# Performance work log

Measured on AMD Instinct MI355X. Metric: run time of the kernel, lower is better.

## Reference

```python
import jax, jax.numpy as jnp
import numpy as np

H, W = 256, 256
S, S_IDX, END_BIAS = 48, 3, 10
E_IDX = S - END_BIAS          # 38
N_ITER = E_IDX - (S_IDX + 1)  # 34 sequential segments after the start segment
OUT_WIN = 10                  # outlier1d window length
OUT_THRESH = 2.0


def setup_inputs() -> dict:
    key = jax.random.key(0)
    # (x, y) event coordinates in [0, W) x [0, H); t/p/b columns are unused by the module.
    events = jax.random.uniform(key, (16, 960000, 2), jnp.float32, minval=0.0, maxval=256.0)
    return {"events": events}


def _blur(a):
    """5x5 uniform (0.04) blur, SAME padding; a: [B, S, D] -> [B, S, D]."""
    k = jnp.full((1, 1, 5, 5), 0.04, jnp.float32)
    return jax.lax.conv_general_dilated(a[:, None], k, (1, 1), [(2, 2), (2, 2)])[:, 0]


def _outlier_flags(m):
    """outlier1d(m[b, si:si+10], thresh=2)[0] for si in [S_IDX+1, E_IDX). m: [B,S] -> bool [B,N_ITER]."""
    widx = (jnp.arange(N_ITER)[:, None] + S_IDX + 1) + jnp.arange(OUT_WIN)[None, :]
    w = m[:, widx]                                   # [B, N_ITER, 10]
    med = jnp.median(w, axis=-1, keepdims=True)
    diff = jnp.abs(w - med)
    mad = jnp.median(diff, axis=-1)                  # [B, N_ITER]
    return 0.6745 * diff[..., 0] / mad > OUT_THRESH


def reference(events):
    B, N, _ = events.shape
    segmentLen = N // S            # static python int
    Nu = segmentLen * S
    x = events[:, :Nu, 0].astype(jnp.int32)   # [B, Nu]
    y = events[:, :Nu, 1].astype(jnp.int32)
    chunks = jnp.repeat(jnp.arange(S), segmentLen)   # segment id per event, [Nu]
    bidx = jnp.arange(B)[:, None]

    # per-batch x-t / y-t histograms via scatter-add
    alongX = jnp.zeros((B, S, W), jnp.float32).at[bidx, chunks[None, :], x].add(1.0)
    alongY = jnp.zeros((B, S, H), jnp.float32).at[bidx, chunks[None, :], y].add(1.0)

    def proc_axis(along, D):
        flat = along.reshape(B, -1)
        cv = (flat.mean(-1) + 3.0 * jnp.std(flat, axis=-1, ddof=1))[:, None, None]
        a = _blur(jnp.clip(along, 0.0, cv))
        m = jnp.einsum('bsd,d->bs', a, jnp.arange(D, dtype=jnp.float32)) / segmentLen
        start = m[:, S_IDX:S_IDX + 1]
        aligned = jnp.round(m - start - (D // 2 - start)).astype(jnp.int32)
        return m, aligned

    meanX, alignedX = proc_axis(alongX, W)
    meanY, alignedY = proc_axis(alongY, H)
    is_out = _outlier_flags(meanX) | _outlier_flags(meanY)   # [B, N_ITER]

    def per_batch(xb, yb, aX, aY, outb):
        xs = jnp.clip(xb - aX[chunks], 0, W - 1)
        ys = jnp.clip(yb - aY[chunks], 0, H - 1)
        idx_c = (xs + W * ys).reshape(S, segmentLen)
        idx_v = (xs // 2 + (W // 2) * (ys // 2)).reshape(S, segmentLen)
        container0 = jnp.zeros(W * H, jnp.int32).at[idx_c[S_IDX]].add(1)
        ver0 = jnp.zeros((W // 2) * (H // 2), bool).at[idx_v[S_IDX]].set(True)

        def step(carry, inp):
            container, ver, stopped = carry
            ic, iv, is_o = inp
            ver_new = ver.at[iv].set(True)
            cnt = jnp.sum(ver_new).astype(jnp.float32)
            new_info = jnp.sum(jnp.logical_xor(ver_new, ver)).astype(jnp.float32)
            brk = new_info / cnt < 0.1
            do = (~stopped) & (~is_o) & (~brk)
            stopped = stopped | ((~stopped) & (~is_o) & brk)
            container = jnp.where(do, container.at[ic].add(1), container)
            ver = jnp.where(do, ver_new, ver)
            return (container, ver, stopped), None

        (container, _, _), _ = jax.lax.scan(
            step, (container0, ver0, jnp.array(False)),
            (idx_c[S_IDX + 1:E_IDX], idx_v[S_IDX + 1:E_IDX], outb))
        c = container.astype(jnp.float32)
        cv = c.mean() + 3.0 * jnp.std(c, ddof=1)
        return jnp.clip(c, 0.0, cv) / cv

    containers = jax.vmap(per_batch)(x, y, alignedX, alignedY, is_out)  # [B, W*H]
    return containers.reshape(B, 1, H, W)
```

## Files before the change

### kernel.cpp

```cpp
#include <hip/hip_runtime.h>

#define NB 16
#define NEV 960000
#define NS 48
#define SEG 20000
#define S_IDX 3
#define E_IDX 38
#define N_ITER 34
#define ND 256
#define NCH 35

__global__ __launch_bounds__(256) void hist_kernel(const float* __restrict__ events,
                                                   float* __restrict__ alongX,
                                                   float* __restrict__ alongY,
                                                   unsigned* __restrict__ compact,
                                                   unsigned* __restrict__ container,
                                                   unsigned* __restrict__ masks,
                                                   unsigned long long* __restrict__ sums,
                                                   unsigned long long* __restrict__ cvsums) {
    __shared__ unsigned hx[4][ND], hy[4][ND];
    __shared__ unsigned long long qredX[4], qredY[4];
    int tid = threadIdx.x;
    int blk = blockIdx.x;
    int b = blk / NS, c = blk % NS;
    int wave = tid >> 6, lane = tid & 63;
    #pragma unroll
    for (int j = 0; j < 4; j++) { hx[j][tid] = 0; hy[j][tid] = 0; }
    {
        uint4 z = {0u, 0u, 0u, 0u};
        for (int i = blk * 256 + tid; i < 262144; i += NB * NS * 256)
            ((uint4*)container)[i] = z;
        for (int i = blk * 256 + tid; i < 71680; i += NB * NS * 256)
            ((uint4*)masks)[i] = z;
        if (blk == 0 && tid < NB * 2) sums[tid] = 0ull;
        if (blk == 1 && tid < NB * 2) cvsums[tid] = 0ull;
    }
    __syncthreads();
    size_t base = (size_t)b * NEV + (size_t)c * SEG;
    const float4* ev4 = (const float4*)(events + base * 2);
    bool wr = (c >= S_IDX && c < E_IDX);
    uint4* dst = wr ? (uint4*)(compact + ((size_t)b * NCH + (c - S_IDX)) * (SEG / 2)) : nullptr;
    unsigned* HX = hx[wave];
    unsigned* HY = hy[wave];
    for (int k = tid; k < SEG / 8; k += 256) {
        float4 v0 = ev4[4 * k], v1 = ev4[4 * k + 1], v2 = ev4[4 * k + 2], v3 = ev4[4 * k + 3];
        int x0 = (int)v0.x, y0 = (int)v0.y, x1 = (int)v0.z, y1 = (int)v0.w;
        int x2 = (int)v1.x, y2 = (int)v1.y, x3 = (int)v1.z, y3 = (int)v1.w;
        int x4 = (int)v2.x, y4 = (int)v2.y, x5 = (int)v2.z, y5 = (int)v2.w;
        int x6 = (int)v3.x, y6 = (int)v3.y, x7 = (int)v3.z, y7 = (int)v3.w;
        x0 = x0 > 255 ? 255 : x0; y0 = y0 > 255 ? 255 : y0;
        x1 = x1 > 255 ? 255 : x1; y1 = y1 > 255 ? 255 : y1;
        x2 = x2 > 255 ? 255 : x2; y2 = y2 > 255 ? 255 : y2;
        x3 = x3 > 255 ? 255 : x3; y3 = y3 > 255 ? 255 : y3;
        x4 = x4 > 255 ? 255 : x4; y4 = y4 > 255 ? 255 : y4;
        x5 = x5 > 255 ? 255 : x5; y5 = y5 > 255 ? 255 : y5;
        x6 = x6 > 255 ? 255 : x6; y6 = y6 > 255 ? 255 : y6;
        x7 = x7 > 255 ? 255 : x7; y7 = y7 > 255 ? 255 : y7;
        atomicAdd(&HX[x0], 1u); atomicAdd(&HY[y0], 1u);
        atomicAdd(&HX[x1], 1u); atomicAdd(&HY[y1], 1u);
        atomicAdd(&HX[x2], 1u); atomicAdd(&HY[y2], 1u);
        atomicAdd(&HX[x3], 1u); atomicAdd(&HY[y3], 1u);
        atomicAdd(&HX[x4], 1u); atomicAdd(&HY[y4], 1u);
        atomicAdd(&HX[x5], 1u); atomicAdd(&HY[y5], 1u);
        atomicAdd(&HX[x6], 1u); atomicAdd(&HY[y6], 1u);
        atomicAdd(&HX[x7], 1u); atomicAdd(&HY[y7], 1u);
        if (wr) {
            uint4 p;
            p.x = (unsigned)(x0 | (y0 << 8)) | ((unsigned)(x1 | (y1 << 8)) << 16);
            p.y = (unsigned)(x2 | (y2 << 8)) | ((unsigned)(x3 | (y3 << 8)) << 16);
            p.z = (unsigned)(x4 | (y4 << 8)) | ((unsigned)(x5 | (y5 << 8)) << 16);
            p.w = (unsigned)(x6 | (y6 << 8)) | ((unsigned)(x7 | (y7 << 8)) << 16);
            dst[k] = p;
        }
    }
    __syncthreads();
    unsigned sx = hx[0][tid] + hx[1][tid] + hx[2][tid] + hx[3][tid];
    unsigned sy = hy[0][tid] + hy[1][tid] + hy[2][tid] + hy[3][tid];
    int o = (b * NS + c) * ND + tid;
    alongX[o] = (float)sx;
    alongY[o] = (float)sy;
    unsigned long long qx = (unsigned long long)sx * sx;
    unsigned long long qy = (unsigned long long)sy * sy;
    for (int off = 32; off; off >>= 1) { qx += __shfl_down(qx, off); qy += __shfl_down(qy, off); }
    if (lane == 0) { qredX[wave] = qx; qredY[wave] = qy; }
    __syncthreads();
    if (tid == 0) {
        atomicAdd(&cvsums[b * 2],     qredX[0] + qredX[1] + qredX[2] + qredX[3]);
        atomicAdd(&cvsums[b * 2 + 1], qredY[0] + qredY[1] + qredY[2] + qredY[3]);
    }
}

__global__ __launch_bounds__(256) void stats_kernel(const float* __restrict__ alongX,
                                                    const float* __restrict__ alongY,
                                                    const unsigned long long* __restrict__ cvsums,
                                                    int* __restrict__ alignedX,
                                                    int* __restrict__ alignedY,
                                                    float* __restrict__ m_all) {
    __shared__ float sbuf[16 * ND];
    int tid = threadIdx.x;
    int blk = blockIdx.x;
    int g = blk & 3, axis = (blk >> 2) & 1, b = blk >> 3;
    const float* along = (axis ? alongY : alongX) + (size_t)b * NS * ND;
    int rbase = g * 12 - 2;
    for (int j = 0; j < 16; j++) {
        int r = rbase + j;
        if (r >= 0 && r < NS) sbuf[j * ND + tid] = along[r * ND + tid];
    }
    double ts  = 960000.0;
    double ts2 = (double)cvsums[b * 2 + axis];
    const double N = (double)(NS * ND);
    double mean = ts / N;
    double var  = (ts2 - ts * ts / N) / (N - 1.0);
    float cv = (float)(mean + 3.0 * sqrt(var));
    __syncthreads();
    int wave = tid >> 6, lane = tid & 63;
    for (int q = 0; q < 3; ++q) {
        int sI = g * 12 + wave * 3 + q;
        double acc = 0.0;
        #pragma unroll
        for (int k = 0; k < 4; ++k) {
            int d = lane + 64 * k;
            int lo = d - 2 < 0 ? 0 : d - 2;
            int hi = d + 2 > 255 ? 255 : d + 2;
            double Wd = 0.5 * (double)(lo + hi) * (double)(hi - lo + 1);
            double t = 0.0;
            #pragma unroll
            for (int ds = -2; ds <= 2; ++ds) {
                int ss = sI + ds;
                if (ss >= 0 && ss < NS) t += (double)fminf(sbuf[(ss - rbase) * ND + d], cv);
            }
            acc += t * Wd;
        }
        for (int off = 32; off; off >>= 1) acc += __shfl_down(acc, off);
        if (lane == 0) {
            float mf = (float)(acc * 0.04 / (double)SEG);
            m_all[(b * 2 + axis) * NS + sI] = mf;
            (axis ? alignedY : alignedX)[b * NS + sI] = (int)rintf(mf - 128.0f);
        }
    }
}

__global__ __launch_bounds__(256) void mask_kernel(const unsigned* __restrict__ compact,
                                                   const int* __restrict__ alignedX,
                                                   const int* __restrict__ alignedY,
                                                   unsigned* __restrict__ masks) {
    __shared__ unsigned sm[512];
    int tid = threadIdx.x, blk = blockIdx.x;
    int hi = blk & 1;
    int tile = blk >> 1;
    int b = tile / NCH, ci = tile % NCH, si = S_IDX + ci;
    sm[tid] = 0; sm[tid + 256] = 0;
    __syncthreads();
    int aX = alignedX[b * NS + si], aY = alignedY[b * NS + si];
    const uint4* cp = (const uint4*)(compact + ((size_t)b * NCH + ci) * (SEG / 2));
    for (int i = hi * 1250 + tid; i < (hi + 1) * 1250; i += 256) {
        uint4 w = cp[i];
        unsigned wsv[4] = {w.x, w.y, w.z, w.w};
        #pragma unroll
        for (int j = 0; j < 4; j++) {
            unsigned v = wsv[j];
            #pragma unroll
            for (int h = 0; h < 2; h++) {
                unsigned e = (h ? (v >> 16) : v) & 0xFFFFu;
                int xs = (int)(e & 255u) - aX; xs = xs < 0 ? 0 : (xs > 255 ? 255 : xs);
                int ys = (int)(e >> 8)   - aY; ys = ys < 0 ? 0 : (ys > 255 ? 255 : ys);
                int iv = (xs >> 1) | ((ys >> 1) << 7);
                atomicOr(&sm[iv >> 5], 1u << (iv & 31));
            }
        }
    }
    __syncthreads();
    unsigned* mo = masks + (size_t)tile * 512;
    unsigned v0 = sm[tid], v1 = sm[tid + 256];
    if (v0) atomicOr(&mo[tid], v0);
    if (v1) atomicOr(&mo[tid + 256], v1);
}

__device__ inline float median10(const float* v) {
    float w[10];
    #pragma unroll
    for (int i = 0; i < 10; i++) w[i] = v[i];
    #pragma unroll
    for (int i = 1; i < 10; i++) {
        float k = w[i]; int j = i - 1;
        while (j >= 0 && w[j] > k) { w[j + 1] = w[j]; j--; }
        w[j + 1] = k;
    }
    return 0.5f * (w[4] + w[5]);
}

__device__ inline bool outlier_flag(const float* w) {
    float med = median10(w);
    float d[10];
    #pragma unroll
    for (int i = 0; i < 10; i++) d[i] = fabsf(w[i] - med);
    float d0 = d[0];
    float mad = median10(d);
    return (0.6745f * d0 / mad) > 2.0f;
}

__device__ inline unsigned wave_sum_u32(unsigned v) {
    for (int off = 32; off; off >>= 1) v += __shfl_xor(v, off);
    return v;
}

__global__ __launch_bounds__(64) void decide_kernel(const unsigned* __restrict__ masks,
                                                    const float* __restrict__ m_all,
                                                    unsigned long long* __restrict__ commitmask) {
    int b = blockIdx.x, lane = threadIdx.x;
    const unsigned* mb = masks + (size_t)b * NCH * 512;
    uint4 v0 = ((const uint4*)mb)[lane * 2];
    uint4 v1 = ((const uint4*)mb)[lane * 2 + 1];
    const uint4* pp = (const uint4*)(mb + 512);
    uint4 p0 = pp[lane * 2], p1 = pp[lane * 2 + 1];
    bool f = false;
    if (lane < N_ITER) {
        const float* mx = m_all + b * 2 * NS;
        const float* my = mx + NS;
        f = outlier_flag(&mx[S_IDX + 1 + lane]) || outlier_flag(&my[S_IDX + 1 + lane]);
    }
    unsigned long long omask = __ballot(f);
    unsigned ver[8] = {v0.x, v0.y, v0.z, v0.w, v1.x, v1.y, v1.z, v1.w};
    unsigned pc = 0;
    #pragma unroll
    for (int j = 0; j < 8; j++) pc += __popc(ver[j]);
    unsigned cnt = wave_sum_u32(pc);
    unsigned long long cm = 1ull;
    for (int idx = 1; idx < NCH; ++idx) {
        uint4 c0 = p0, c1 = p1;
        if (idx + 1 < NCH) {
            const uint4* np = (const uint4*)(mb + (size_t)(idx + 1) * 512);
            p0 = np[lane * 2]; p1 = np[lane * 2 + 1];
        }
        unsigned del[8] = {c0.x, c0.y, c0.z, c0.w, c1.x, c1.y, c1.z, c1.w};
        unsigned nl = 0;
        #pragma unroll
        for (int j = 0; j < 8; j++) nl += __popc(del[j] & ~ver[j]);
        unsigned ni = wave_sum_u32(nl);
        bool is_o = (omask >> (idx - 1)) & 1;
        if (!is_o) {
            unsigned cn = cnt + ni;
            float ratio = (float)ni / (float)cn;
            if (ratio < 0.1f) break;
            cm |= 1ull << idx;
            cnt = cn;
            #pragma unroll
            for (int j = 0; j < 8; j++) ver[j] |= del[j];
        }
    }
    if (lane == 0) commitmask[b] = cm;
}

__global__ __launch_bounds__(256) void commit_kernel(const unsigned* __restrict__ compact,
                                                     const int* __restrict__ alignedX,
                                                     const int* __restrict__ alignedY,
                                                     const unsigned long long* __restrict__ commitmask,
                                                     unsigned* __restrict__ container) {
    int blk = blockIdx.x, tid = threadIdx.x;
    int qi = blk & 3;
    int tile = blk >> 2;
    int b = tile / NCH, ci = tile % NCH;
    if (!((commitmask[b] >> ci) & 1ull)) return;
    int si = S_IDX + ci;
    int aX = alignedX[b * NS + si], aY = alignedY[b * NS + si];
    unsigned* cont = container + (size_t)b * 65536;
    const uint4* cp = (const uint4*)(compact + ((size_t)b * NCH + ci) * (SEG / 2));
    for (int i = qi * 625 + tid; i < (qi + 1) * 625; i += 256) {
        uint4 w = cp[i];
        unsigned wsv[4] = {w.x, w.y, w.z, w.w};
        #pragma unroll
        for (int j = 0; j < 4; j++) {
            unsigned v = wsv[j];
            #pragma unroll
            for (int h = 0; h < 2; h++) {
                unsigned e = (h ? (v >> 16) : v) & 0xFFFFu;
                int xs = (int)(e & 255u) - aX; xs = xs < 0 ? 0 : (xs > 255 ? 255 : xs);
                int ys = (int)(e >> 8)   - aY; ys = ys < 0 ? 0 : (ys > 255 ? 255 : ys);
                atomicAdd(&cont[xs | (ys << 8)], 1u);
            }
        }
    }
}

__global__ __launch_bounds__(256) void cv_kernel(const unsigned* __restrict__ container,
                                                 unsigned long long* __restrict__ sums) {
    __shared__ unsigned long long sredA[4], sredB[4];
    int tid = threadIdx.x, blk = blockIdx.x;
    int b = blk >> 4, part = blk & 15;
    const uint4* c4 = (const uint4*)(container + (size_t)b * 65536) + part * 1024;
    unsigned long long s = 0, s2 = 0;
    for (int i = tid; i < 1024; i += 256) {
        uint4 v = c4[i];
        s  += (unsigned long long)v.x + v.y + v.z + v.w;
        s2 += (unsigned long long)v.x * v.x + (unsigned long long)v.y * v.y
            + (unsigned long long)v.z * v.z + (unsigned long long)v.w * v.w;
    }
    for (int off = 32; off; off >>= 1) { s += __shfl_down(s, off); s2 += __shfl_down(s2, off); }
    if ((tid & 63) == 0) { sredA[tid >> 6] = s; sredB[tid >> 6] = s2; }
    __syncthreads();
    if (tid == 0) {
        atomicAdd(&sums[b * 2],     sredA[0] + sredA[1] + sredA[2] + sredA[3]);
        atomicAdd(&sums[b * 2 + 1], sredB[0] + sredB[1] + sredB[2] + sredB[3]);
    }
}

__global__ __launch_bounds__(256) void finish_kernel(const unsigned* __restrict__ container,
                                                     const unsigned long long* __restrict__ sums,
                                                     float* __restrict__ out) {
    int g = blockIdx.x * 256 + threadIdx.x;
    int b = g >> 14;
    double ts  = (double)sums[b * 2];
    double ts2 = (double)sums[b * 2 + 1];
    double mean = ts / 65536.0;
    double var  = (ts2 - ts * ts / 65536.0) / 65535.0;
    float cv = (float)(mean + 3.0 * sqrt(var));
    uint4 v = ((const uint4*)container)[g];
    float4 o;
    o.x = fminf((float)v.x, cv) / cv;
    o.y = fminf((float)v.y, cv) / cv;
    o.z = fminf((float)v.z, cv) / cv;
    o.w = fminf((float)v.w, cv) / cv;
    ((float4*)out)[g] = o;
}

extern "C" void kernel_launch(void* const* d_in, const int* in_sizes, int n_in,
                              void* d_out, int out_size, void* d_ws, size_t ws_size,
                              hipStream_t stream) {
    const float* events = (const float*)d_in[0];
    float* out = (float*)d_out;
    char* ws = (char*)d_ws;

    float*    alongX    = (float*)(ws);
    float*    alongY    = (float*)(ws + 786432);
    unsigned* container = (unsigned*)(ws + 1572864);
    int*      alignedX  = (int*)(ws + 5767168);
    int*      alignedY  = (int*)(ws + 5770240);
    float*    m_all     = (float*)(ws + 5773312);
    unsigned long long* commitmask = (unsigned long long*)(ws + 5779456);
    unsigned long long* sums       = (unsigned long long*)(ws + 5779584);
    unsigned long long* cvsums     = (unsigned long long*)(ws + 5779840);
    unsigned* compact   = (unsigned*)(ws + 6291456);
    unsigned* masks     = (unsigned*)(ws + 29360128);

    hist_kernel<<<NB * NS, 256, 0, stream>>>(events, alongX, alongY, compact,
                                             container, masks, sums, cvsums);
    stats_kernel<<<NB * 2 * 4, 256, 0, stream>>>(alongX, alongY, cvsums,
                                                 alignedX, alignedY, m_all);
    mask_kernel<<<NB * NCH * 2, 256, 0, stream>>>(compact, alignedX, alignedY, masks);
    decide_kernel<<<NB, 64, 0, stream>>>(masks, m_all, commitmask);
    commit_kernel<<<NB * NCH * 4, 256, 0, stream>>>(compact, alignedX, alignedY,
                                                    commitmask, container);
    cv_kernel<<<NB * 16, 256, 0, stream>>>(container, sums);
    finish_kernel<<<1024, 256, 0, stream>>>(container, sums, out);
}
```

Before: 269.4 us.

## Fuse all seven pipeline kernels into one cooperative persistent kernel with grid syncs

Replaces the seven separate kernel launches with a single cooperative mega-kernel of 768 blocks. Stages are separated by grid.sync(), and shared memory is reused through a union. The aim is to remove per-launch overhead and inter-kernel gaps, which matter here because several stages are tiny. In exchange the grid is fixed at 768 blocks, so some stages now loop over virtual blocks, and the many grid-wide barriers add their own synchronisation cost.

After: 841.5 us. 212% more time.

```diff
diff --git a/kernel.cpp b/kernel.cpp
--- a/kernel.cpp
+++ b/kernel.cpp
@@ -1,4 +1,7 @@
 #include <hip/hip_runtime.h>
+#include <hip/hip_cooperative_groups.h>
+
+namespace cg = cooperative_groups;
 
 #define NB 16
 #define NEV 960000
@@ -9,172 +12,7 @@
 #define N_ITER 34
 #define ND 256
 #define NCH 35
-
-__global__ __launch_bounds__(256) void hist_kernel(const float* __restrict__ events,
-                                                   float* __restrict__ alongX,
-                                                   float* __restrict__ alongY,
-                                                   unsigned* __restrict__ compact,
-                                                   unsigned* __restrict__ container,
-                                                   unsigned* __restrict__ masks,
-                                                   unsigned long long* __restrict__ sums,
-                                                   unsigned long long* __restrict__ cvsums) {
-    __shared__ unsigned hx[4][ND], hy[4][ND];
-    __shared__ unsigned long long qredX[4], qredY[4];
-    int tid = threadIdx.x;
-    int blk = blockIdx.x;
-    int b = blk / NS, c = blk % NS;
-    int wave = tid >> 6, lane = tid & 63;
-    #pragma unroll
-    for (int j = 0; j < 4; j++) { hx[j][tid] = 0; hy[j][tid] = 0; }
-    {
-        uint4 z = {0u, 0u, 0u, 0u};
-        for (int i = blk * 256 + tid; i < 262144; i += NB * NS * 256)
-            ((uint4*)container)[i] = z;
-        for (int i = blk * 256 + tid; i < 71680; i += NB * NS * 256)
-            ((uint4*)masks)[i] = z;
-        if (blk == 0 && tid < NB * 2) sums[tid] = 0ull;
-        if (blk == 1 && tid < NB * 2) cvsums[tid] = 0ull;
-    }
-    __syncthreads();
-    size_t base = (size_t)b * NEV + (size_t)c * SEG;
-    const float4* ev4 = (const float4*)(events + base * 2);
-    bool wr = (c >= S_IDX && c < E_IDX);
-    uint4* dst = wr ? (uint4*)(compact + ((size_t)b * NCH + (c - S_IDX)) * (SEG / 2)) : nullptr;
-    unsigned* HX = hx[wave];
-    unsigned* HY = hy[wave];
-    for (int k = tid; k < SEG / 8; k += 256) {
-        float4 v0 = ev4[4 * k], v1 = ev4[4 * k + 1], v2 = ev4[4 * k + 2], v3 = ev4[4 * k + 3];
-        int x0 = (int)v0.x, y0 = (int)v0.y, x1 = (int)v0.z, y1 = (int)v0.w;
-        int x2 = (int)v1.x, y2 = (int)v1.y, x3 = (int)v1.z, y3 = (int)v1.w;
-        int x4 = (int)v2.x, y4 = (int)v2.y, x5 = (int)v2.z, y5 = (int)v2.w;
-        int x6 = (int)v3.x, y6 = (int)v3.y, x7 = (int)v3.z, y7 = (int)v3.w;
-        x0 = x0 > 255 ? 255 : x0; y0 = y0 > 255 ? 255 : y0;
-        x1 = x1 > 255 ? 255 : x1; y1 = y1 > 255 ? 255 : y1;
-        x2 = x2 > 255 ? 255 : x2; y2 = y2 > 255 ? 255 : y2;
-        x3 = x3 > 255 ? 255 : x3; y3 = y3 > 255 ? 255 : y3;
-        x4 = x4 > 255 ? 255 : x4; y4 = y4 > 255 ? 255 : y4;
-        x5 = x5 > 255 ? 255 : x5; y5 = y5 > 255 ? 255 : y5;
-        x6 = x6 > 255 ? 255 : x6; y6 = y6 > 255 ? 255 : y6;
-        x7 = x7 > 255 ? 255 : x7; y7 = y7 > 255 ? 255 : y7;
-        atomicAdd(&HX[x0], 1u); atomicAdd(&HY[y0], 1u);
-        atomicAdd(&HX[x1], 1u); atomicAdd(&HY[y1], 1u);
-        atomicAdd(&HX[x2], 1u); atomicAdd(&HY[y2], 1u);
-        atomicAdd(&HX[x3], 1u); atomicAdd(&HY[y3], 1u);
-        atomicAdd(&HX[x4], 1u); atomicAdd(&HY[y4], 1u);
-        atomicAdd(&HX[x5], 1u); atomicAdd(&HY[y5], 1u);
-        atomicAdd(&HX[x6], 1u); atomicAdd(&HY[y6], 1u);
-        atomicAdd(&HX[x7], 1u); atomicAdd(&HY[y7], 1u);
-        if (wr) {
-            uint4 p;
-            p.x = (unsigned)(x0 | (y0 << 8)) | ((unsigned)(x1 | (y1 << 8)) << 16);
-            p.y = (unsigned)(x2 | (y2 << 8)) | ((unsigned)(x3 | (y3 << 8)) << 16);
-            p.z = (unsigned)(x4 | (y4 << 8)) | ((unsigned)(x5 | (y5 << 8)) << 16);
-            p.w = (unsigned)(x6 | (y6 << 8)) | ((unsigned)(x7 | (y7 << 8)) << 16);
-            dst[k] = p;
-        }
-    }
-    __syncthreads();
-    unsigned sx = hx[0][tid] + hx[1][tid] + hx[2][tid] + hx[3][tid];
-    unsigned sy = hy[0][tid] + hy[1][tid] + hy[2][tid] + hy[3][tid];
-    int o = (b * NS + c) * ND + tid;
-    alongX[o] = (float)sx;
-    alongY[o] = (float)sy;
-    unsigned long long qx = (unsigned long long)sx * sx;
-    unsigned long long qy = (unsigned long long)sy * sy;
-    for (int off = 32; off; off >>= 1) { qx += __shfl_down(qx, off); qy += __shfl_down(qy, off); }
-    if (lane == 0) { qredX[wave] = qx; qredY[wave] = qy; }
-    __syncthreads();
-    if (tid == 0) {
-        atomicAdd(&cvsums[b * 2],     qredX[0] + qredX[1] + qredX[2] + qredX[3]);
-        atomicAdd(&cvsums[b * 2 + 1], qredY[0] + qredY[1] + qredY[2] + qredY[3]);
-    }
-}
-
-__global__ __launch_bounds__(256) void stats_kernel(const float* __restrict__ alongX,
-                                                    const float* __restrict__ alongY,
-                                                    const unsigned long long* __restrict__ cvsums,
-                                                    int* __restrict__ alignedX,
-                                                    int* __restrict__ alignedY,
-                                                    float* __restrict__ m_all) {
-    __shared__ float sbuf[16 * ND];
-    int tid = threadIdx.x;
-    int blk = blockIdx.x;
-    int g = blk & 3, axis = (blk >> 2) & 1, b = blk >> 3;
-    const float* along = (axis ? alongY : alongX) + (size_t)b * NS * ND;
-    int rbase = g * 12 - 2;
-    for (int j = 0; j < 16; j++) {
-        int r = rbase + j;
-        if (r >= 0 && r < NS) sbuf[j * ND + tid] = along[r * ND + tid];
-    }
-    double ts  = 960000.0;
-    double ts2 = (double)cvsums[b * 2 + axis];
-    const double N = (double)(NS * ND);
-    double mean = ts / N;
-    double var  = (ts2 - ts * ts / N) / (N - 1.0);
-    float cv = (float)(mean + 3.0 * sqrt(var));
-    __syncthreads();
-    int wave = tid >> 6, lane = tid & 63;
-    for (int q = 0; q < 3; ++q) {
-        int sI = g * 12 + wave * 3 + q;
-        double acc = 0.0;
-        #pragma unroll
-        for (int k = 0; k < 4; ++k) {
-            int d = lane + 64 * k;
-            int lo = d - 2 < 0 ? 0 : d - 2;
-            int hi = d + 2 > 255 ? 255 : d + 2;
-            double Wd = 0.5 * (double)(lo + hi) * (double)(hi - lo + 1);
-            double t = 0.0;
-            #pragma unroll
-            for (int ds = -2; ds <= 2; ++ds) {
-                int ss = sI + ds;
-                if (ss >= 0 && ss < NS) t += (double)fminf(sbuf[(ss - rbase) * ND + d], cv);
-            }
-            acc += t * Wd;
-        }
-        for (int off = 32; off; off >>= 1) acc += __shfl_down(acc, off);
-        if (lane == 0) {
-            float mf = (float)(acc * 0.04 / (double)SEG);
-            m_all[(b * 2 + axis) * NS + sI] = mf;
-            (axis ? alignedY : alignedX)[b * NS + sI] = (int)rintf(mf - 128.0f);
-        }
-    }
-}
-
-__global__ __launch_bounds__(256) void mask_kernel(const unsigned* __restrict__ compact,
-                                                   const int* __restrict__ alignedX,
-                                                   const int* __restrict__ alignedY,
-                                                   unsigned* __restrict__ masks) {
-    __shared__ unsigned sm[512];
-    int tid = threadIdx.x, blk = blockIdx.x;
-    int hi = blk & 1;
-    int tile = blk >> 1;
-    int b = tile / NCH, ci = tile % NCH, si = S_IDX + ci;
-    sm[tid] = 0; sm[tid + 256] = 0;
-    __syncthreads();
-    int aX = alignedX[b * NS + si], aY = alignedY[b * NS + si];
-    const uint4* cp = (const uint4*)(compact + ((size_t)b * NCH + ci) * (SEG / 2));
-    for (int i = hi * 1250 + tid; i < (hi + 1) * 1250; i += 256) {
-        uint4 w = cp[i];
-        unsigned wsv[4] = {w.x, w.y, w.z, w.w};
-        #pragma unroll
-        for (int j = 0; j < 4; j++) {
-            unsigned v = wsv[j];
-            #pragma unroll
-            for (int h = 0; h < 2; h++) {
-                unsigned e = (h ? (v >> 16) : v) & 0xFFFFu;
-                int xs = (int)(e & 255u) - aX; xs = xs < 0 ? 0 : (xs > 255 ? 255 : xs);
-                int ys = (int)(e >> 8)   - aY; ys = ys < 0 ? 0 : (ys > 255 ? 255 : ys);
-                int iv = (xs >> 1) | ((ys >> 1) << 7);
-                atomicOr(&sm[iv >> 5], 1u << (iv & 31));
-            }
-        }
-    }
-    __syncthreads();
-    unsigned* mo = masks + (size_t)tile * 512;
-    unsigned v0 = sm[tid], v1 = sm[tid + 256];
-    if (v0) atomicOr(&mo[tid], v0);
-    if (v1) atomicOr(&mo[tid + 256], v1);
-}
+#define GRID 768
 
 __device__ inline float median10(const float* v) {
     float w[10];
@@ -204,132 +42,9 @@
     return v;
 }
 
-__global__ __launch_bounds__(64) void decide_kernel(const unsigned* __restrict__ masks,
-                                                    const float* __restrict__ m_all,
-                                                    unsigned long long* __restrict__ commitmask) {
-    int b = blockIdx.x, lane = threadIdx.x;
-    const unsigned* mb = masks + (size_t)b * NCH * 512;
-    uint4 v0 = ((const uint4*)mb)[lane * 2];
-    uint4 v1 = ((const uint4*)mb)[lane * 2 + 1];
-    const uint4* pp = (const uint4*)(mb + 512);
-    uint4 p0 = pp[lane * 2], p1 = pp[lane * 2 + 1];
-    bool f = false;
-    if (lane < N_ITER) {
-        const float* mx = m_all + b * 2 * NS;
-        const float* my = mx + NS;
-        f = outlier_flag(&mx[S_IDX + 1 + lane]) || outlier_flag(&my[S_IDX + 1 + lane]);
-    }
-    unsigned long long omask = __ballot(f);
-    unsigned ver[8] = {v0.x, v0.y, v0.z, v0.w, v1.x, v1.y, v1.z, v1.w};
-    unsigned pc = 0;
-    #pragma unroll
-    for (int j = 0; j < 8; j++) pc += __popc(ver[j]);
-    unsigned cnt = wave_sum_u32(pc);
-    unsigned long long cm = 1ull;
-    for (int idx = 1; idx < NCH; ++idx) {
-        uint4 c0 = p0, c1 = p1;
-        if (idx + 1 < NCH) {
-            const uint4* np = (const uint4*)(mb + (size_t)(idx + 1) * 512);
-            p0 = np[lane * 2]; p1 = np[lane * 2 + 1];
-        }
-        unsigned del[8] = {c0.x, c0.y, c0.z, c0.w, c1.x, c1.y, c1.z, c1.w};
-        unsigned nl = 0;
-        #pragma unroll
-        for (int j = 0; j < 8; j++) nl += __popc(del[j] & ~ver[j]);
-        unsigned ni = wave_sum_u32(nl);
-        bool is_o = (omask >> (idx - 1)) & 1;
-        if (!is_o) {
-            unsigned cn = cnt + ni;
-            float ratio = (float)ni / (float)cn;
-            if (ratio < 0.1f) break;
-            cm |= 1ull << idx;
-            cnt = cn;
-            #pragma unroll
-            for (int j = 0; j < 8; j++) ver[j] |= del[j];
-        }
-    }
-    if (lane == 0) commitmask[b] = cm;
-}
-
-__global__ __launch_bounds__(256) void commit_kernel(const unsigned* __restrict__ compact,
-                                                     const int* __restrict__ alignedX,
-                                                     const int* __restrict__ alignedY,
-                                                     const unsigned long long* __restrict__ commitmask,
-                                                     unsigned* __restrict__ container) {
-    int blk = blockIdx.x, tid = threadIdx.x;
-    int qi = blk & 3;
-    int tile = blk >> 2;
-    int b = tile / NCH, ci = tile % NCH;
-    if (!((commitmask[b] >> ci) & 1ull)) return;
-    int si = S_IDX + ci;
-    int aX = alignedX[b * NS + si], aY = alignedY[b * NS + si];
-    unsigned* cont = container + (size_t)b * 65536;
-    const uint4* cp = (const uint4*)(compact + ((size_t)b * NCH + ci) * (SEG / 2));
-    for (int i = qi * 625 + tid; i < (qi + 1) * 625; i += 256) {
-        uint4 w = cp[i];
-        unsigned wsv[4] = {w.x, w.y, w.z, w.w};
-        #pragma unroll
-        for (int j = 0; j < 4; j++) {
-            unsigned v = wsv[j];
-            #pragma unroll
-            for (int h = 0; h < 2; h++) {
-                unsigned e = (h ? (v >> 16) : v) & 0xFFFFu;
-                int xs = (int)(e & 255u) - aX; xs = xs < 0 ? 0 : (xs > 255 ? 255 : xs);
-                int ys = (int)(e >> 8)   - aY; ys = ys < 0 ? 0 : (ys > 255 ? 255 : ys);
-                atomicAdd(&cont[xs | (ys << 8)], 1u);
-            }
-        }
-    }
-}
-
-__global__ __launch_bounds__(256) void cv_kernel(const unsigned* __restrict__ container,
-                                                 unsigned long long* __restrict__ sums) {
-    __shared__ unsigned long long sredA[4], sredB[4];
-    int tid = threadIdx.x, blk = blockIdx.x;
-    int b = blk >> 4, part = blk & 15;
-    const uint4* c4 = (const uint4*)(container + (size_t)b * 65536) + part * 1024;
-    unsigned long long s = 0, s2 = 0;
-    for (int i = tid; i < 1024; i += 256) {
-        uint4 v = c4[i];
-        s  += (unsigned long long)v.x + v.y + v.z + v.w;
-        s2 += (unsigned long long)v.x * v.x + (unsigned long long)v.y * v.y
-            + (unsigned long long)v.z * v.z + (unsigned long long)v.w * v.w;
-    }
-    for (int off = 32; off; off >>= 1) { s += __shfl_down(s, off); s2 += __shfl_down(s2, off); }
-    if ((tid & 63) == 0) { sredA[tid >> 6] = s; sredB[tid >> 6] = s2; }
-    __syncthreads();
-    if (tid == 0) {
-        atomicAdd(&sums[b * 2],     sredA[0] + sredA[1] + sredA[2] + sredA[3]);
-        atomicAdd(&sums[b * 2 + 1], sredB[0] + sredB[1] + sredB[2] + sredB[3]);
-    }
-}
-
-__global__ __launch_bounds__(256) void finish_kernel(const unsigned* __restrict__ container,
-                                                     const unsigned long long* __restrict__ sums,
-                                                     float* __restrict__ out) {
-    int g = blockIdx.x * 256 + threadIdx.x;
-    int b = g >> 14;
-    double ts  = (double)sums[b * 2];
-    double ts2 = (double)sums[b * 2 + 1];
-    double mean = ts / 65536.0;
-    double var  = (ts2 - ts * ts / 65536.0) / 65535.0;
-    float cv = (float)(mean + 3.0 * sqrt(var));
-    uint4 v = ((const uint4*)container)[g];
-    float4 o;
-    o.x = fminf((float)v.x, cv) / cv;
-    o.y = fminf((float)v.y, cv) / cv;
-    o.z = fminf((float)v.z, cv) / cv;
-    o.w = fminf((float)v.w, cv) / cv;
-    ((float4*)out)[g] = o;
-}
-
-extern "C" void kernel_launch(void* const* d_in, const int* in_sizes, int n_in,
-                              void* d_out, int out_size, void* d_ws, size_t ws_size,
-                              hipStream_t stream) {
-    const float* events = (const float*)d_in[0];
-    float* out = (float*)d_out;
-    char* ws = (char*)d_ws;
-
+__global__ __launch_bounds__(256, 3) void mega_kernel(const float* __restrict__ events,
+                                                      char* __restrict__ ws,
+                                                      float* __restrict__ out) {
     float*    alongX    = (float*)(ws);
     float*    alongY    = (float*)(ws + 786432);
     unsigned* container = (unsigned*)(ws + 1572864);
@@ -342,14 +57,282 @@
     unsigned* compact   = (unsigned*)(ws + 6291456);
     unsigned* masks     = (unsigned*)(ws + 29360128);
 
-    hist_kernel<<<NB * NS, 256, 0, stream>>>(events, alongX, alongY, compact,
-                                             container, masks, sums, cvsums);
-    stats_kernel<<<NB * 2 * 4, 256, 0, stream>>>(alongX, alongY, cvsums,
-                                                 alignedX, alignedY, m_all);
-    mask_kernel<<<NB * NCH * 2, 256, 0, stream>>>(compact, alignedX, alignedY, masks);
-    decide_kernel<<<NB, 64, 0, stream>>>(masks, m_all, commitmask);
-    commit_kernel<<<NB * NCH * 4, 256, 0, stream>>>(compact, alignedX, alignedY,
-                                                    commitmask, container);
-    cv_kernel<<<NB * 16, 256, 0, stream>>>(container, sums);
-    finish_kernel<<<1024, 256, 0, stream>>>(container, sums, out);
-}
+    __shared__ union {
+        struct { unsigned hx[4][ND], hy[4][ND]; unsigned long long qredX[4], qredY[4]; } h;
+        struct { float sbuf[16 * ND]; } s;
+        struct { unsigned sm[512]; } m;
+        struct { unsigned long long a[4], b2[4]; } c;
+    } u;
+
+    cg::grid_group grid = cg::this_grid();
+    int tid = threadIdx.x;
+    int blk = blockIdx.x;
+    int wave = tid >> 6, lane = tid & 63;
+
+    {
+        uint4 z = {0u, 0u, 0u, 0u};
+        for (int i = blk * 256 + tid; i < 262144; i += GRID * 256)
+            ((uint4*)container)[i] = z;
+        for (int i = blk * 256 + tid; i < 71680; i += GRID * 256)
+            ((uint4*)masks)[i] = z;
+        if (blk == 0 && tid < NB * 2) { sums[tid] = 0ull; cvsums[tid] = 0ull; }
+    }
+    grid.sync();
+
+    {
+        int b = blk / NS, c = blk % NS;
+        #pragma unroll
+        for (int j = 0; j < 4; j++) { u.h.hx[j][tid] = 0; u.h.hy[j][tid] = 0; }
+        __syncthreads();
+        size_t base = (size_t)b * NEV + (size_t)c * SEG;
+        const float4* ev4 = (const float4*)(events + base * 2);
+        bool wr = (c >= S_IDX && c < E_IDX);
+        uint4* dst = wr ? (uint4*)(compact + ((size_t)b * NCH + (c - S_IDX)) * (SEG / 2)) : nullptr;
+        unsigned* HX = u.h.hx[wave];
+        unsigned* HY = u.h.hy[wave];
+        for (int k = tid; k < SEG / 8; k += 256) {
+            float4 v0 = ev4[4 * k], v1 = ev4[4 * k + 1], v2 = ev4[4 * k + 2], v3 = ev4[4 * k + 3];
+            int x0 = (int)v0.x, y0 = (int)v0.y, x1 = (int)v0.z, y1 = (int)v0.w;
+            int x2 = (int)v1.x, y2 = (int)v1.y, x3 = (int)v1.z, y3 = (int)v1.w;
+            int x4 = (int)v2.x, y4 = (int)v2.y, x5 = (int)v2.z, y5 = (int)v2.w;
+            int x6 = (int)v3.x, y6 = (int)v3.y, x7 = (int)v3.z, y7 = (int)v3.w;
+            x0 = x0 > 255 ? 255 : x0; y0 = y0 > 255 ? 255 : y0;
+            x1 = x1 > 255 ? 255 : x1; y1 = y1 > 255 ? 255 : y1;
+            x2 = x2 > 255 ? 255 : x2; y2 = y2 > 255 ? 255 : y2;
+            x3 = x3 > 255 ? 255 : x3; y3 = y3 > 255 ? 255 : y3;
+            x4 = x4 > 255 ? 255 : x4; y4 = y4 > 255 ? 255 : y4;
+            x5 = x5 > 255 ? 255 : x5; y5 = y5 > 255 ? 255 : y5;
+            x6 = x6 > 255 ? 255 : x6; y6 = y6 > 255 ? 255 : y6;
+            x7 = x7 > 255 ? 255 : x7; y7 = y7 > 255 ? 255 : y7;
+            atomicAdd(&HX[x0], 1u); atomicAdd(&HY[y0], 1u);
+            atomicAdd(&HX[x1], 1u); atomicAdd(&HY[y1], 1u);
+            atomicAdd(&HX[x2], 1u); atomicAdd(&HY[y2], 1u);
+            atomicAdd(&HX[x3], 1u); atomicAdd(&HY[y3], 1u);
+            atomicAdd(&HX[x4], 1u); atomicAdd(&HY[y4], 1u);
+            atomicAdd(&HX[x5], 1u); atomicAdd(&HY[y5], 1u);
+            atomicAdd(&HX[x6], 1u); atomicAdd(&HY[y6], 1u);
+            atomicAdd(&HX[x7], 1u); atomicAdd(&HY[y7], 1u);
+            if (wr) {
+                uint4 p;
+                p.x = (unsigned)(x0 | (y0 << 8)) | ((unsigned)(x1 | (y1 << 8)) << 16);
+                p.y = (unsigned)(x2 | (y2 << 8)) | ((unsigned)(x3 | (y3 << 8)) << 16);
+                p.z = (unsigned)(x4 | (y4 << 8)) | ((unsigned)(x5 | (y5 << 8)) << 16);
+                p.w = (unsigned)(x6 | (y6 << 8)) | ((unsigned)(x7 | (y7 << 8)) << 16);
+                dst[k] = p;
+            }
+        }
+        __syncthreads();
+        unsigned sx = u.h.hx[0][tid] + u.h.hx[1][tid] + u.h.hx[2][tid] + u.h.hx[3][tid];
+        unsigned sy = u.h.hy[0][tid] + u.h.hy[1][tid] + u.h.hy[2][tid] + u.h.hy[3][tid];
+        int o = (b * NS + c) * ND + tid;
+        alongX[o] = (float)sx;
+        alongY[o] = (float)sy;
+        unsigned long long qx = (unsigned long long)sx * sx;
+        unsigned long long qy = (unsigned long long)sy * sy;
+        for (int off = 32; off; off >>= 1) { qx += __shfl_down(qx, off); qy += __shfl_down(qy, off); }
+        if (lane == 0) { u.h.qredX[wave] = qx; u.h.qredY[wave] = qy; }
+        __syncthreads();
+        if (tid == 0) {
+            atomicAdd(&cvsums[b * 2],     u.h.qredX[0] + u.h.qredX[1] + u.h.qredX[2] + u.h.qredX[3]);
+            atomicAdd(&cvsums[b * 2 + 1], u.h.qredY[0] + u.h.qredY[1] + u.h.qredY[2] + u.h.qredY[3]);
+        }
+    }
+    grid.sync();
+
+    if (blk < NB * 2 * 4) {
+        int g = blk & 3, axis = (blk >> 2) & 1, b = blk >> 3;
+        const float* along = (axis ? alongY : alongX) + (size_t)b * NS * ND;
+        int rbase = g * 12 - 2;
+        for (int j = 0; j < 16; j++) {
+            int r = rbase + j;
+            if (r >= 0 && r < NS) u.s.sbuf[j * ND + tid] = along[r * ND + tid];
+        }
+        double ts  = 960000.0;
+        double ts2 = (double)cvsums[b * 2 + axis];
+        const double N = (double)(NS * ND);
+        double mean = ts / N;
+        double var  = (ts2 - ts * ts / N) / (N - 1.0);
+        float cv = (float)(mean + 3.0 * sqrt(var));
+        __syncthreads();
+        for (int q = 0; q < 3; ++q) {
+            int sI = g * 12 + wave * 3 + q;
+            double acc = 0.0;
+            #pragma unroll
+            for (int k = 0; k < 4; ++k) {
+                int d = lane + 64 * k;
+                int lo = d - 2 < 0 ? 0 : d - 2;
+                int hi = d + 2 > 255 ? 255 : d + 2;
+                double Wd = 0.5 * (double)(lo + hi) * (double)(hi - lo + 1);
+                double t = 0.0;
+                #pragma unroll
+                for (int ds = -2; ds <= 2; ++ds) {
+                    int ss = sI + ds;
+                    if (ss >= 0 && ss < NS) t += (double)fminf(u.s.sbuf[(ss - rbase) * ND + d], cv);
+                }
+                acc += t * Wd;
+            }
+            for (int off = 32; off; off >>= 1) acc += __shfl_down(acc, off);
+            if (lane == 0) {
+                float mf = (float)(acc * 0.04 / (double)SEG);
+                m_all[(b * 2 + axis) * NS + sI] = mf;
+                (axis ? alignedY : alignedX)[b * NS + sI] = (int)rintf(mf - 128.0f);
+            }
+        }
+    }
+    grid.sync();
+
+    for (int vb = blk; vb < NB * NCH * 2; vb += GRID) {
+        int hi = vb & 1;
+        int tile = vb >> 1;
+        int b = tile / NCH, ci = tile % NCH, si = S_IDX + ci;
+        u.m.sm[tid] = 0; u.m.sm[tid + 256] = 0;
+        __syncthreads();
+        int aX = alignedX[b * NS + si], aY = alignedY[b * NS + si];
+        const uint4* cp = (const uint4*)(compact + ((size_t)b * NCH + ci) * (SEG / 2));
+        for (int i = hi * 1250 + tid; i < (hi + 1) * 1250; i += 256) {
+            uint4 w = cp[i];
+            unsigned wsv[4] = {w.x, w.y, w.z, w.w};
+            #pragma unroll
+            for (int j = 0; j < 4; j++) {
+                unsigned v = wsv[j];
+                #pragma unroll
+                for (int h = 0; h < 2; h++) {
+                    unsigned e = (h ? (v >> 16) : v) & 0xFFFFu;
+                    int xs = (int)(e & 255u) - aX; xs = xs < 0 ? 0 : (xs > 255 ? 255 : xs);
+                    int ys = (int)(e >> 8)   - aY; ys = ys < 0 ? 0 : (ys > 255 ? 255 : ys);
+                    int iv = (xs >> 1) | ((ys >> 1) << 7);
+                    atomicOr(&u.m.sm[iv >> 5], 1u << (iv & 31));
+                }
+            }
+        }
+        __syncthreads();
+        unsigned* mo = masks + (size_t)tile * 512;
+        unsigned v0 = u.m.sm[tid], v1 = u.m.sm[tid + 256];
+        if (v0) atomicOr(&mo[tid], v0);
+        if (v1) atomicOr(&mo[tid + 256], v1);
+    }
+    grid.sync();
+
+    if (blk < NB && tid < 64) {
+        int b = blk;
+        const unsigned* mb = masks + (size_t)b * NCH * 512;
+        uint4 v0 = ((const uint4*)mb)[lane * 2];
+        uint4 v1 = ((const uint4*)mb)[lane * 2 + 1];
+        const uint4* pp = (const uint4*)(mb + 512);
+        uint4 p0 = pp[lane * 2], p1 = pp[lane * 2 + 1];
+        bool f = false;
+        if (lane < N_ITER) {
+            const float* mx = m_all + b * 2 * NS;
+            const float* my = mx + NS;
+            f = outlier_flag(&mx[S_IDX + 1 + lane]) || outlier_flag(&my[S_IDX + 1 + lane]);
+        }
+        unsigned long long omask = __ballot(f);
+        unsigned ver[8] = {v0.x, v0.y, v0.z, v0.w, v1.x, v1.y, v1.z, v1.w};
+        unsigned pc = 0;
+        #pragma unroll
+        for (int j = 0; j < 8; j++) pc += __popc(ver[j]);
+        unsigned cnt = wave_sum_u32(pc);
+        unsigned long long cm = 1ull;
+        for (int idx = 1; idx < NCH; ++idx) {
+            uint4 c0 = p0, c1 = p1;
+            if (idx + 1 < NCH) {
+                const uint4* np = (const uint4*)(mb + (size_t)(idx + 1) * 512);
+                p0 = np[lane * 2]; p1 = np[lane * 2 + 1];
+            }
+            unsigned del[8] = {c0.x, c0.y, c0.z, c0.w, c1.x, c1.y, c1.z, c1.w};
+            unsigned nl = 0;
+            #pragma unroll
+            for (int j = 0; j < 8; j++) nl += __popc(del[j] & ~ver[j]);
+            unsigned ni = wave_sum_u32(nl);
+            bool is_o = (omask >> (idx - 1)) & 1;
+            if (!is_o) {
+                unsigned cn = cnt + ni;
+                float ratio = (float)ni / (float)cn;
+                if (ratio < 0.1f) break;
+                cm |= 1ull << idx;
+                cnt = cn;
+                #pragma unroll
+                for (int j = 0; j < 8; j++) ver[j] |= del[j];
+            }
+        }
+        if (lane == 0) commitmask[b] = cm;
+    }
+    grid.sync();
+
+    for (int vb = blk; vb < NB * NCH * 4; vb += GRID) {
+        int qi = vb & 3;
+        int tile = vb >> 2;
+        int b = tile / NCH, ci = tile % NCH;
+        if (!((commitmask[b] >> ci) & 1ull)) continue;
+        int si = S_IDX + ci;
+        int aX = alignedX[b * NS + si], aY = alignedY[b * NS + si];
+        unsigned* cont = container + (size_t)b * 65536;
+        const uint4* cp = (const uint4*)(compact + ((size_t)b * NCH + ci) * (SEG / 2));
+        for (int i = qi * 625 + tid; i < (qi + 1) * 625; i += 256) {
+            uint4 w = cp[i];
+            unsigned wsv[4] = {w.x, w.y, w.z, w.w};
+            #pragma unroll
+            for (int j = 0; j < 4; j++) {
+                unsigned v = wsv[j];
+                #pragma unroll
+                for (int h = 0; h < 2; h++) {
+                    unsigned e = (h ? (v >> 16) : v) & 0xFFFFu;
+                    int xs = (int)(e & 255u) - aX; xs = xs < 0 ? 0 : (xs > 255 ? 255 : xs);
+                    int ys = (int)(e >> 8)   - aY; ys = ys < 0 ? 0 : (ys > 255 ? 255 : ys);
+                    atomicAdd(&cont[xs | (ys << 8)], 1u);
+                }
+            }
+        }
+    }
+    grid.sync();
+
+    if (blk < NB * 16) {
+        int b = blk >> 4, part = blk & 15;
+        const uint4* c4 = (const uint4*)(container + (size_t)b * 65536) + part * 1024;
+        unsigned long long s = 0, s2 = 0;
+        for (int i = tid; i < 1024; i += 256) {
+            uint4 v = c4[i];
+            s  += (unsigned long long)v.x + v.y + v.z + v.w;
+            s2 += (unsigned long long)v.x * v.x + (unsigned long long)v.y * v.y
+                + (unsigned long long)v.z * v.z + (unsigned long long)v.w * v.w;
+        }
+        for (int off = 32; off; off >>= 1) { s += __shfl_down(s, off); s2 += __shfl_down(s2, off); }
+        if ((tid & 63) == 0) { u.c.a[tid >> 6] = s; u.c.b2[tid >> 6] = s2; }
+        __syncthreads();
+        if (tid == 0) {
+            atomicAdd(&sums[b * 2],     u.c.a[0] + u.c.a[1] + u.c.a[2] + u.c.a[3]);
+            atomicAdd(&sums[b * 2 + 1], u.c.b2[0] + u.c.b2[1] + u.c.b2[2] + u.c.b2[3]);
+        }
+    }
+    grid.sync();
+
+    for (int g = blk * 256 + tid; g < 262144; g += GRID * 256) {
+        int b = g >> 14;
+        double ts  = (double)sums[b * 2];
+        double ts2 = (double)sums[b * 2 + 1];
+        double mean = ts / 65536.0;
+        double var  = (ts2 - ts * ts / 65536.0) / 65535.0;
+        float cv = (float)(mean + 3.0 * sqrt(var));
+        uint4 v = ((const uint4*)container)[g];
+        float4 o;
+        o.x = fminf((float)v.x, cv) / cv;
+        o.y = fminf((float)v.y, cv) / cv;
+        o.z = fminf((float)v.z, cv) / cv;
+        o.w = fminf((float)v.w, cv) / cv;
+        ((float4*)out)[g] = o;
+    }
+}
+
+extern "C" void kernel_launch(void* const* d_in, const int* in_sizes, int n_in,
+                              void* d_out, int out_size, void* d_ws, size_t ws_size,
+                              hipStream_t stream) {
+    const float* events = (const float*)d_in[0];
+    float* out = (float*)d_out;
+    char* ws = (char*)d_ws;
+    void* args[3];
+    args[0] = (void*)&events;
+    args[1] = (void*)&ws;
+    args[2] = (void*)&out;
+    hipLaunchCooperativeKernel((const void*)mega_kernel, dim3(GRID), dim3(256),
+                               args, 0, stream);
+}
```
